# Optimization experiments

Measured on AMD Instinct MI355X. Metric: run time of the kernel, lower is better.

## Reference

```python
import jax, jax.numpy as jnp
import numpy as np

N, E, DIN, HID, DOUT = 50000, 800000, 128, 128, 64
NEG_SLOPE = 0.2


def setup_inputs() -> dict:
    key = jax.random.key(0)
    ks = jax.random.split(key, 16)
    x = jax.random.normal(ks[0], (N, DIN), dtype=jnp.float32)
    edge_index = jax.random.randint(ks[1], (2, E), 0, N, dtype=jnp.int64)

    def lin(k, fan_in, fan_out):
        kw, kb = jax.random.split(k)
        s = 1.0 / np.sqrt(fan_in)
        W = jax.random.uniform(kw, (fan_in, fan_out), jnp.float32, -s, s)
        b = jax.random.uniform(kb, (fan_out,), jnp.float32, -s, s)
        return W, b

    Wl, bl = lin(ks[2], DIN, DIN)   # GATv2 lin_l
    Wr, br = lin(ks[3], DIN, DIN)   # GATv2 lin_r
    att = jax.random.uniform(ks[4], (DIN,), jnp.float32, -1.0 / np.sqrt(DIN), 1.0 / np.sqrt(DIN))
    bg = jnp.zeros((DIN,), jnp.float32)  # GAT output bias
    W1, b1 = lin(ks[5], DIN, HID)   # ChebConv K=1 -> plain linear
    W2, b2 = lin(ks[6], HID, HID)
    W3, b3 = lin(ks[7], HID, DOUT)
    return {"x": x, "edge_index": edge_index, "Wl": Wl, "bl": bl, "Wr": Wr,
            "br": br, "att": att, "bg": bg, "W1": W1, "b1": b1,
            "W2": W2, "b2": b2, "W3": W3, "b3": b3}


def reference(x, edge_index, Wl, bl, Wr, br, att, bg, W1, b1, W2, b2, W3, b3):
    n = x.shape[0]
    # GATv2Conv adds self loops by default
    loop = jnp.arange(n, dtype=edge_index.dtype)
    src = jnp.concatenate([edge_index[0], loop])  # source j
    dst = jnp.concatenate([edge_index[1], loop])  # target i

    xl = x @ Wl + bl  # [N, DIN]
    xr = x @ Wr + br  # [N, DIN]

    # GATv2 edge scores: leaky_relu(x_l[j] + x_r[i]) . att
    e = jax.nn.leaky_relu(xl[src] + xr[dst], NEG_SLOPE)  # [E+N, DIN]
    a = e @ att                                          # [E+N]

    # softmax over incoming edges of each destination node
    amax = jax.ops.segment_max(a, dst, num_segments=n)
    ea = jnp.exp(a - amax[dst])
    denom = jax.ops.segment_sum(ea, dst, num_segments=n)
    alpha = ea / denom[dst]                              # [E+N]

    # aggregate messages alpha * x_l[j] at destinations
    h = jax.ops.segment_sum(alpha[:, None] * xl[src], dst, num_segments=n) + bg

    # ChebConv with K=1 reduces to a linear layer (T_0(L) = I)
    h = jax.nn.relu(h @ W1 + b1)
    h = jax.nn.relu(h @ W2 + b2)
    # dropout_rate = 0.0 -> identity
    return h @ W3 + b3
```

## Files before the change

### kernel.cpp

```cpp
#include <hip/hip_runtime.h>
#include <hip/hip_bf16.h>

#define DIN 128
#define NEG_SLOPE 0.2f
#define PTILE 2048
#define FCAP 8192
#define CVT_BLKS 289

typedef __attribute__((ext_vector_type(8))) short bf16x8;
typedef __attribute__((ext_vector_type(8))) unsigned short u16x8;
typedef __attribute__((ext_vector_type(4))) float f32x4;

__device__ __forceinline__ ushort f2bf(float f) {
  unsigned u = __float_as_uint(f);
  u += 0x7FFFu + ((u >> 16) & 1u);
  return (ushort)(u >> 16);
}
__device__ __forceinline__ float bf2f(ushort u) {
  return __uint_as_float((unsigned)u << 16);
}

__global__ __launch_bounds__(256) void cvt_hist_kernel(
    const float* __restrict__ Wl, const float* __restrict__ Wr,
    const float* __restrict__ W1, const float* __restrict__ W2,
    const float* __restrict__ W3,
    ushort* __restrict__ WlT, ushort* __restrict__ WrT,
    ushort* __restrict__ W1T, ushort* __restrict__ W2T,
    ushort* __restrict__ W3T,
    const int* __restrict__ ei, int* __restrict__ ghist, int E) {
  if (blockIdx.x < CVT_BLKS) {
    int i = blockIdx.x * 256 + threadIdx.x;
    if (i < 16384) {
      int k = i >> 7, c = i & 127; WlT[c * 128 + k] = f2bf(Wl[i]);
    } else if (i < 32768) {
      int j = i - 16384; int k = j >> 7, c = j & 127; WrT[c * 128 + k] = f2bf(Wr[j]);
    } else if (i < 49152) {
      int j = i - 32768; int k = j >> 7, c = j & 127; W1T[c * 128 + k] = f2bf(W1[j]);
    } else if (i < 65536) {
      int j = i - 49152; int k = j >> 7, c = j & 127; W2T[c * 128 + k] = f2bf(W2[j]);
    } else if (i < 73728) {
      int j = i - 65536; int k = j >> 6, c = j & 63; W3T[c * 128 + k] = f2bf(W3[j]);
    }
  } else {
    __shared__ int h[256];
    h[threadIdx.x] = 0;
    __syncthreads();
    int tile = blockIdx.x - CVT_BLKS;
    for (int e = tile * PTILE + threadIdx.x;
         e < min(E, (tile + 1) * PTILE); e += 256)
      atomicAdd(&h[ei[E + e] >> 8], 1);
    __syncthreads();
    if (h[threadIdx.x] > 0) atomicAdd(&ghist[threadIdx.x], h[threadIdx.x]);
  }
}

__global__ __launch_bounds__(256) void lin_lr_mfma_kernel(
    const float* __restrict__ x,
    const ushort* __restrict__ WlT, const float* __restrict__ bl,
    const ushort* __restrict__ WrT, const float* __restrict__ br,
    ushort* __restrict__ xl, ushort* __restrict__ xr, int n) {
  const int tid = threadIdx.x;
  const int wv = tid >> 6, lane = tid & 63;
  const int m = lane & 15, quad = lane >> 4;
  const int colbase = (wv & 1) * 64;
  const int nodew = blockIdx.x * 32 + (wv >> 1) * 16;
  int arow = nodew + m; if (arow >= n) arow = n - 1;
  f32x4 accl[4], accr[4];
#pragma unroll
  for (int nt = 0; nt < 4; nt++) { accl[nt] = (f32x4){0,0,0,0}; accr[nt] = (f32x4){0,0,0,0}; }
#pragma unroll
  for (int kk = 0; kk < 4; kk++) {
    int k0 = kk * 32 + quad * 8;
    const float4* xp = (const float4*)(x + (long)arow * 128 + k0);
    float4 x0 = xp[0], x1 = xp[1];
    bf16x8 af;
    af[0] = (short)f2bf(x0.x); af[1] = (short)f2bf(x0.y);
    af[2] = (short)f2bf(x0.z); af[3] = (short)f2bf(x0.w);
    af[4] = (short)f2bf(x1.x); af[5] = (short)f2bf(x1.y);
    af[6] = (short)f2bf(x1.z); af[7] = (short)f2bf(x1.w);
#pragma unroll
    for (int nt = 0; nt < 4; nt++) {
      int brow = colbase + nt * 16 + m;
      bf16x8 bl8 = *(const bf16x8*)(WlT + brow * 128 + k0);
      bf16x8 br8 = *(const bf16x8*)(WrT + brow * 128 + k0);
      accl[nt] = __builtin_amdgcn_mfma_f32_16x16x32_bf16(af, bl8, accl[nt], 0, 0, 0);
      accr[nt] = __builtin_amdgcn_mfma_f32_16x16x32_bf16(af, br8, accr[nt], 0, 0, 0);
    }
  }
#pragma unroll
  for (int nt = 0; nt < 4; nt++) {
    int col = colbase + nt * 16 + m;
    float vbl = bl[col], vbr = br[col];
#pragma unroll
    for (int r = 0; r < 4; r++) {
      int node = nodew + quad * 4 + r;
      if (node < n) {
        xl[(long)node * 128 + col] = f2bf(accl[nt][r] + vbl);
        xr[(long)node * 128 + col] = f2bf(accr[nt][r] + vbr);
      }
    }
  }
}

__global__ __launch_bounds__(256) void scan_small_kernel(
    const int* __restrict__ ghist, int* __restrict__ cum,
    int* __restrict__ cursor) {
  __shared__ int sh[256];
  int tid = threadIdx.x;
  int v = ghist[tid];
  sh[tid] = v;
  __syncthreads();
  for (int d = 1; d < 256; d <<= 1) {
    int t = (tid >= d) ? sh[tid - d] : 0;
    __syncthreads();
    sh[tid] += t;
    __syncthreads();
  }
  int exc = sh[tid] - v;
  cum[tid] = exc;
  cursor[tid] = exc;
  if (tid == 255) cum[256] = sh[255];
}

__global__ __launch_bounds__(256) void partition_kernel(
    const int* __restrict__ ei, unsigned* __restrict__ part,
    int* __restrict__ cursor, int E) {
  __shared__ int hist[256], pref[256], sexcl[256], curs[256], gbase[256];
  __shared__ unsigned buf[PTILE];
  const int tid = threadIdx.x;
  const int tile0 = blockIdx.x * PTILE;
  const int tcount = min(PTILE, E - tile0);
  hist[tid] = 0;
  __syncthreads();
  unsigned pk[PTILE / 256];
  int cnt = 0;
  for (int i = tid; i < tcount; i += 256) {
    int e = tile0 + i;
    int s = ei[e], d = ei[E + e];
    unsigned p = ((unsigned)d << 16) | (unsigned)s;
    pk[cnt++] = p;
    atomicAdd(&hist[d >> 8], 1);
  }
  __syncthreads();
  int v = hist[tid];
  pref[tid] = v;
  __syncthreads();
  for (int d = 1; d < 256; d <<= 1) {
    int t = (tid >= d) ? pref[tid - d] : 0;
    __syncthreads();
    pref[tid] += t;
    __syncthreads();
  }
  int exc = pref[tid] - v;
  sexcl[tid] = exc;
  curs[tid] = exc;
  gbase[tid] = (v > 0) ? atomicAdd(&cursor[tid], v) : 0;
  __syncthreads();
  for (int j = 0; j < cnt; j++) {
    int b = pk[j] >> 24;
    int pos = atomicAdd(&curs[b], 1);
    buf[pos] = pk[j];
  }
  __syncthreads();
  for (int i = tid; i < tcount; i += 256) {
    unsigned p = buf[i];
    int b = p >> 24;
    part[gbase[b] + (i - sexcl[b])] = p;
  }
}

__global__ __launch_bounds__(512) void fine_kernel(
    const unsigned* __restrict__ part, const int* __restrict__ cum,
    int* __restrict__ offsets, int* __restrict__ ssrc,
    int N, int E, int nbuck) {
  __shared__ int hist[256], pref[256], curs[256];
  __shared__ unsigned buf[FCAP], buf2[FCAP];
  const int tid = threadIdx.x;
  const int b = blockIdx.x;
  const int seg0 = cum[b];
  const int len = min(cum[b + 1] - seg0, FCAP);
  if (tid < 256) hist[tid] = 0;
  __syncthreads();
  for (int i = tid; i < len; i += 512) {
    unsigned p = part[seg0 + i];
    buf[i] = p;
    atomicAdd(&hist[(p >> 16) & 255], 1);
  }
  __syncthreads();
  int v = (tid < 256) ? hist[tid] : 0;
  if (tid < 256) pref[tid] = v;
  __syncthreads();
  for (int d = 1; d < 256; d <<= 1) {
    int t = (tid >= d && tid < 256) ? pref[tid - d] : 0;
    __syncthreads();
    if (tid < 256) pref[tid] += t;
    __syncthreads();
  }
  if (tid < 256) {
    int exc = pref[tid] - v;
    curs[tid] = exc;
    int node = b * 256 + tid;
    if (node < N) offsets[node] = seg0 + exc;
  }
  if (b == nbuck - 1 && tid == 0) offsets[N] = E;
  __syncthreads();
  for (int i = tid; i < len; i += 512) {
    unsigned p = buf[i];
    int pos = atomicAdd(&curs[(p >> 16) & 255], 1);
    buf2[pos] = p;
  }
  __syncthreads();
  for (int i = tid; i < len; i += 512)
    ssrc[seg0 + i] = (int)(buf2[i] & 0xFFFFu);
}

__global__ __launch_bounds__(256) void node_aggr_kernel(
    const ushort* __restrict__ xl, const ushort* __restrict__ xr,
    const float* __restrict__ att, const float* __restrict__ bg,
    const int* __restrict__ offsets, const int* __restrict__ ssrc,
    ushort* __restrict__ h, int n) {
  int wave = (int)((blockIdx.x * (long)blockDim.x + threadIdx.x) >> 6);
  int lane = threadIdx.x & 63;
  if (wave >= n) return;
  const int node = wave;
  const int eg = lane >> 4, sl = lane & 15;
  float av[8], r[8], acc[8];
  {
    const float4* ap = (const float4*)(att + sl * 8);
    float4 a0 = ap[0], a1 = ap[1];
    av[0]=a0.x; av[1]=a0.y; av[2]=a0.z; av[3]=a0.w;
    av[4]=a1.x; av[5]=a1.y; av[6]=a1.z; av[7]=a1.w;
  }
  bf16x8 rv = *(const bf16x8*)(xr + (long)node * 128 + sl * 8);
#pragma unroll
  for (int j = 0; j < 8; j++) r[j] = bf2f((ushort)rv[j]);
  bf16x8 lv = *(const bf16x8*)(xl + (long)node * 128 + sl * 8);
  float denom;
  {
    float t = 0.f;
    float l[8];
#pragma unroll
    for (int j = 0; j < 8; j++) {
      l[j] = bf2f((ushort)lv[j]);
      float v = l[j] + r[j];
      v = fmaxf(v, NEG_SLOPE * v);
      t = fmaf(v, av[j], t);
    }
#pragma unroll
    for (int off = 1; off < 16; off <<= 1) t += __shfl_xor(t, off);
    float es = __expf(t);
    denom = (eg == 0) ? es : 0.f;
#pragma unroll
    for (int j = 0; j < 8; j++) acc[j] = (eg == 0) ? es * l[j] : 0.f;
  }
  const int beg = offsets[node];
  const int end = offsets[node + 1];
  for (int p = beg; p < end; p += 8) {
    int ia = p + eg, ib = p + 4 + eg;
    bool va = ia < end, vb = ib < end;
    int sa = va ? ssrc[ia] : node;
    int sb = vb ? ssrc[ib] : node;
    bf16x8 uva = *(const bf16x8*)(xl + (long)sa * 128 + sl * 8);
    bf16x8 uvb = *(const bf16x8*)(xl + (long)sb * 128 + sl * 8);
    float ua[8], ub[8], ta = 0.f, tb = 0.f;
#pragma unroll
    for (int j = 0; j < 8; j++) {
      ua[j] = bf2f((ushort)uva[j]);
      ub[j] = bf2f((ushort)uvb[j]);
      float wa = ua[j] + r[j]; wa = fmaxf(wa, NEG_SLOPE * wa);
      float wb = ub[j] + r[j]; wb = fmaxf(wb, NEG_SLOPE * wb);
      ta = fmaf(wa, av[j], ta);
      tb = fmaf(wb, av[j], tb);
    }
#pragma unroll
    for (int off = 1; off < 16; off <<= 1) {
      ta += __shfl_xor(ta, off);
      tb += __shfl_xor(tb, off);
    }
    float ea = va ? __expf(ta) : 0.f;
    float eb = vb ? __expf(tb) : 0.f;
    denom += ea + eb;
#pragma unroll
    for (int j = 0; j < 8; j++)
      acc[j] = fmaf(eb, ub[j], fmaf(ea, ua[j], acc[j]));
  }
#pragma unroll
  for (int j = 0; j < 8; j++) {
    acc[j] += __shfl_xor(acc[j], 16);
    acc[j] += __shfl_xor(acc[j], 32);
  }
  denom += __shfl_xor(denom, 16);
  denom += __shfl_xor(denom, 32);
  if (eg == 0) {
    float inv = 1.0f / denom;
    const float4* bp = (const float4*)(bg + sl * 8);
    float4 g0 = bp[0], g1 = bp[1];
    float gv[8] = {g0.x, g0.y, g0.z, g0.w, g1.x, g1.y, g1.z, g1.w};
    u16x8 o;
#pragma unroll
    for (int j = 0; j < 8; j++) o[j] = f2bf(fmaf(acc[j], inv, gv[j]));
    *(u16x8*)(h + (long)node * 128 + sl * 8) = o;
  }
}

#define LDSP 136
__global__ __launch_bounds__(256) void mlp_mfma_kernel(
    const ushort* __restrict__ hb,
    const ushort* __restrict__ W1T, const float* __restrict__ b1,
    const ushort* __restrict__ W2T, const float* __restrict__ b2,
    const ushort* __restrict__ W3T, const float* __restrict__ b3,
    float* __restrict__ out, int n) {
  __shared__ ushort act[32][LDSP];
  const int tid = threadIdx.x;
  const int wv = tid >> 6, lane = tid & 63;
  const int m = lane & 15, quad = lane >> 4;
  const int half = wv & 1, ng = wv >> 1;
  const int colbase = half * 64;
  const int nodew = blockIdx.x * 32 + ng * 16;
  int arow = nodew + m; if (arow >= n) arow = n - 1;
  f32x4 acc[4];
#pragma unroll
  for (int nt = 0; nt < 4; nt++) acc[nt] = (f32x4){0,0,0,0};
#pragma unroll
  for (int kk = 0; kk < 4; kk++) {
    int k0 = kk * 32 + quad * 8;
    bf16x8 af = *(const bf16x8*)(hb + (long)arow * 128 + k0);
#pragma unroll
    for (int nt = 0; nt < 4; nt++) {
      bf16x8 b8 = *(const bf16x8*)(W1T + (colbase + nt * 16 + m) * 128 + k0);
      acc[nt] = __builtin_amdgcn_mfma_f32_16x16x32_bf16(af, b8, acc[nt], 0, 0, 0);
    }
  }
#pragma unroll
  for (int nt = 0; nt < 4; nt++) {
    int col = colbase + nt * 16 + m;
    float b = b1[col];
#pragma unroll
    for (int r = 0; r < 4; r++)
      act[ng * 16 + quad * 4 + r][col] = f2bf(fmaxf(acc[nt][r] + b, 0.f));
  }
  __syncthreads();
#pragma unroll
  for (int nt = 0; nt < 4; nt++) acc[nt] = (f32x4){0,0,0,0};
#pragma unroll
  for (int kk = 0; kk < 4; kk++) {
    int k0 = kk * 32 + quad * 8;
    bf16x8 af = *(const bf16x8*)(&act[ng * 16 + m][k0]);
#pragma unroll
    for (int nt = 0; nt < 4; nt++) {
      bf16x8 b8 = *(const bf16x8*)(W2T + (colbase + nt * 16 + m) * 128 + k0);
      acc[nt] = __builtin_amdgcn_mfma_f32_16x16x32_bf16(af, b8, acc[nt], 0, 0, 0);
    }
  }
  __syncthreads();
#pragma unroll
  for (int nt = 0; nt < 4; nt++) {
    int col = colbase + nt * 16 + m;
    float b = b2[col];
#pragma unroll
    for (int r = 0; r < 4; r++)
      act[ng * 16 + quad * 4 + r][col] = f2bf(fmaxf(acc[nt][r] + b, 0.f));
  }
  __syncthreads();
  f32x4 acc3[2];
#pragma unroll
  for (int nt = 0; nt < 2; nt++) acc3[nt] = (f32x4){0,0,0,0};
#pragma unroll
  for (int kk = 0; kk < 4; kk++) {
    int k0 = kk * 32 + quad * 8;
    bf16x8 af = *(const bf16x8*)(&act[ng * 16 + m][k0]);
#pragma unroll
    for (int nt = 0; nt < 2; nt++) {
      bf16x8 b8 = *(const bf16x8*)(W3T + (half * 32 + nt * 16 + m) * 128 + k0);
      acc3[nt] = __builtin_amdgcn_mfma_f32_16x16x32_bf16(af, b8, acc3[nt], 0, 0, 0);
    }
  }
#pragma unroll
  for (int nt = 0; nt < 2; nt++) {
    int col = half * 32 + nt * 16 + m;
    float b = b3[col];
#pragma unroll
    for (int r = 0; r < 4; r++) {
      int node = nodew + quad * 4 + r;
      if (node < n) out[(long)node * 64 + col] = acc3[nt][r] + b;
    }
  }
}

extern "C" void kernel_launch(void* const* d_in, const int* in_sizes, int n_in,
                              void* d_out, int out_size, void* d_ws, size_t ws_size,
                              hipStream_t stream) {
  const float* x   = (const float*)d_in[0];
  const int*   ei  = (const int*)d_in[1];
  const float* Wl  = (const float*)d_in[2];
  const float* bl  = (const float*)d_in[3];
  const float* Wr  = (const float*)d_in[4];
  const float* br  = (const float*)d_in[5];
  const float* att = (const float*)d_in[6];
  const float* bg  = (const float*)d_in[7];
  const float* W1  = (const float*)d_in[8];
  const float* b1  = (const float*)d_in[9];
  const float* W2  = (const float*)d_in[10];
  const float* b2  = (const float*)d_in[11];
  const float* W3  = (const float*)d_in[12];
  const float* b3  = (const float*)d_in[13];
  float* out = (float*)d_out;

  const int N = in_sizes[0] / DIN;
  const int E = in_sizes[1] / 2;
  const int nbuck = (N + 255) >> 8;

  char* ws = (char*)d_ws;
  size_t off = 0;
  int* ghist    = (int*)(ws + off);    off += 256 * 4;
  int* cum      = (int*)(ws + off);    off += 257 * 4;
  int* cursor   = (int*)(ws + off);    off += 256 * 4;
  int* offsets  = (int*)(ws + off);    off += ((size_t)N + 4) * 4;
  unsigned* part= (unsigned*)(ws + off); off += (size_t)E * 4;
  int* ssrc     = (int*)(ws + off);    off += (size_t)E * 4;
  ushort* xlb   = (ushort*)(ws + off); off += (size_t)N * DIN * 2;
  ushort* xrb   = (ushort*)(ws + off); off += (size_t)N * DIN * 2;
  ushort* hbf   = (ushort*)(ws + off); off += (size_t)N * DIN * 2;
  ushort* WlT   = (ushort*)(ws + off); off += 16384 * 2;
  ushort* WrT   = (ushort*)(ws + off); off += 16384 * 2;
  ushort* W1T   = (ushort*)(ws + off); off += 16384 * 2;
  ushort* W2T   = (ushort*)(ws + off); off += 16384 * 2;
  ushort* W3T   = (ushort*)(ws + off); off += 8192 * 2;
  (void)ws_size;

  hipMemsetAsync(ghist, 0, 256 * 4, stream);

  int ntile = (E + PTILE - 1) / PTILE;
  cvt_hist_kernel<<<CVT_BLKS + ntile, 256, 0, stream>>>(
      Wl, Wr, W1, W2, W3, WlT, WrT, W1T, W2T, W3T, ei, ghist, E);

  int nblk32 = (N + 31) / 32;
  lin_lr_mfma_kernel<<<nblk32, 256, 0, stream>>>(x, WlT, bl, WrT, br,
                                                 xlb, xrb, N);

  scan_small_kernel<<<1, 256, 0, stream>>>(ghist, cum, cursor);
  partition_kernel<<<ntile, 256, 0, stream>>>(ei, part, cursor, E);
  fine_kernel<<<nbuck, 512, 0, stream>>>(part, cum, offsets, ssrc, N, E, nbuck);

  int nwblk = (N + 3) / 4;
  node_aggr_kernel<<<nwblk, 256, 0, stream>>>(xlb, xrb, att, bg,
                                              offsets, ssrc, hbf, N);

  mlp_mfma_kernel<<<nblk32, 256, 0, stream>>>(hbf, W1T, b1, W2T, b2,
                                              W3T, b3, out, N);
}
```

Measured before the change: 251.7 us.

## Fuse linear projection with edge partition; shrink source indices; pack aggregation math

Merges the GATv2 lin_l/lin_r MFMA kernel and the edge partition kernel into one launch, with block ranges split by index, so the two independent jobs run concurrently and one launch is removed. Sorted source indices are stored as 16-bit values instead of 32-bit, halving that traffic in fine_kernel and node_aggr. The aggregation kernel converts bf16 in pairs, uses two-wide float vector arithmetic, and has each 16-lane edge group take two consecutive edges. The workspace allocator now aligns every buffer to 256 bytes; the 16-bit indices assume N is at most 65536.

Result: faster. 242.1 us (-3.8%).

```diff
diff --git a/kernel.cpp b/kernel.cpp
--- a/kernel.cpp
+++ b/kernel.cpp
@@ -10,6 +10,8 @@
 typedef __attribute__((ext_vector_type(8))) short bf16x8;
 typedef __attribute__((ext_vector_type(8))) unsigned short u16x8;
 typedef __attribute__((ext_vector_type(4))) float f32x4;
+typedef __attribute__((ext_vector_type(2))) float f32x2;
+typedef __attribute__((ext_vector_type(4))) unsigned int u32x4;
 
 __device__ __forceinline__ ushort f2bf(float f) {
   unsigned u = __float_as_uint(f);
@@ -18,6 +20,12 @@
 }
 __device__ __forceinline__ float bf2f(ushort u) {
   return __uint_as_float((unsigned)u << 16);
+}
+__device__ __forceinline__ f32x2 bfpair(unsigned u) {
+  f32x2 r;
+  r.x = __uint_as_float(u << 16);
+  r.y = __uint_as_float(u & 0xFFFF0000u);
+  return r;
 }
 
 __global__ __launch_bounds__(256) void cvt_hist_kernel(
@@ -54,54 +62,6 @@
   }
 }
 
-__global__ __launch_bounds__(256) void lin_lr_mfma_kernel(
-    const float* __restrict__ x,
-    const ushort* __restrict__ WlT, const float* __restrict__ bl,
-    const ushort* __restrict__ WrT, const float* __restrict__ br,
-    ushort* __restrict__ xl, ushort* __restrict__ xr, int n) {
-  const int tid = threadIdx.x;
-  const int wv = tid >> 6, lane = tid & 63;
-  const int m = lane & 15, quad = lane >> 4;
-  const int colbase = (wv & 1) * 64;
-  const int nodew = blockIdx.x * 32 + (wv >> 1) * 16;
-  int arow = nodew + m; if (arow >= n) arow = n - 1;
-  f32x4 accl[4], accr[4];
-#pragma unroll
-  for (int nt = 0; nt < 4; nt++) { accl[nt] = (f32x4){0,0,0,0}; accr[nt] = (f32x4){0,0,0,0}; }
-#pragma unroll
-  for (int kk = 0; kk < 4; kk++) {
-    int k0 = kk * 32 + quad * 8;
-    const float4* xp = (const float4*)(x + (long)arow * 128 + k0);
-    float4 x0 = xp[0], x1 = xp[1];
-    bf16x8 af;
-    af[0] = (short)f2bf(x0.x); af[1] = (short)f2bf(x0.y);
-    af[2] = (short)f2bf(x0.z); af[3] = (short)f2bf(x0.w);
-    af[4] = (short)f2bf(x1.x); af[5] = (short)f2bf(x1.y);
-    af[6] = (short)f2bf(x1.z); af[7] = (short)f2bf(x1.w);
-#pragma unroll
-    for (int nt = 0; nt < 4; nt++) {
-      int brow = colbase + nt * 16 + m;
-      bf16x8 bl8 = *(const bf16x8*)(WlT + brow * 128 + k0);
-      bf16x8 br8 = *(const bf16x8*)(WrT + brow * 128 + k0);
-      accl[nt] = __builtin_amdgcn_mfma_f32_16x16x32_bf16(af, bl8, accl[nt], 0, 0, 0);
-      accr[nt] = __builtin_amdgcn_mfma_f32_16x16x32_bf16(af, br8, accr[nt], 0, 0, 0);
-    }
-  }
-#pragma unroll
-  for (int nt = 0; nt < 4; nt++) {
-    int col = colbase + nt * 16 + m;
-    float vbl = bl[col], vbr = br[col];
-#pragma unroll
-    for (int r = 0; r < 4; r++) {
-      int node = nodew + quad * 4 + r;
-      if (node < n) {
-        xl[(long)node * 128 + col] = f2bf(accl[nt][r] + vbl);
-        xr[(long)node * 128 + col] = f2bf(accr[nt][r] + vbr);
-      }
-    }
-  }
-}
-
 __global__ __launch_bounds__(256) void scan_small_kernel(
     const int* __restrict__ ghist, int* __restrict__ cum,
     int* __restrict__ cursor) {
@@ -122,56 +82,104 @@
   if (tid == 255) cum[256] = sh[255];
 }
 
-__global__ __launch_bounds__(256) void partition_kernel(
+__global__ __launch_bounds__(256) void lin_partition_kernel(
+    const float* __restrict__ x,
+    const ushort* __restrict__ WlT, const float* __restrict__ bl,
+    const ushort* __restrict__ WrT, const float* __restrict__ br,
+    ushort* __restrict__ xl, ushort* __restrict__ xr, int n, int nblk_lin,
     const int* __restrict__ ei, unsigned* __restrict__ part,
     int* __restrict__ cursor, int E) {
-  __shared__ int hist[256], pref[256], sexcl[256], curs[256], gbase[256];
-  __shared__ unsigned buf[PTILE];
-  const int tid = threadIdx.x;
-  const int tile0 = blockIdx.x * PTILE;
-  const int tcount = min(PTILE, E - tile0);
-  hist[tid] = 0;
-  __syncthreads();
-  unsigned pk[PTILE / 256];
-  int cnt = 0;
-  for (int i = tid; i < tcount; i += 256) {
-    int e = tile0 + i;
-    int s = ei[e], d = ei[E + e];
-    unsigned p = ((unsigned)d << 16) | (unsigned)s;
-    pk[cnt++] = p;
-    atomicAdd(&hist[d >> 8], 1);
-  }
-  __syncthreads();
-  int v = hist[tid];
-  pref[tid] = v;
-  __syncthreads();
-  for (int d = 1; d < 256; d <<= 1) {
-    int t = (tid >= d) ? pref[tid - d] : 0;
-    __syncthreads();
-    pref[tid] += t;
-    __syncthreads();
-  }
-  int exc = pref[tid] - v;
-  sexcl[tid] = exc;
-  curs[tid] = exc;
-  gbase[tid] = (v > 0) ? atomicAdd(&cursor[tid], v) : 0;
-  __syncthreads();
-  for (int j = 0; j < cnt; j++) {
-    int b = pk[j] >> 24;
-    int pos = atomicAdd(&curs[b], 1);
-    buf[pos] = pk[j];
-  }
-  __syncthreads();
-  for (int i = tid; i < tcount; i += 256) {
-    unsigned p = buf[i];
-    int b = p >> 24;
-    part[gbase[b] + (i - sexcl[b])] = p;
+  if ((int)blockIdx.x < nblk_lin) {
+    const int tid = threadIdx.x;
+    const int wv = tid >> 6, lane = tid & 63;
+    const int m = lane & 15, quad = lane >> 4;
+    const int colbase = (wv & 1) * 64;
+    const int nodew = blockIdx.x * 32 + (wv >> 1) * 16;
+    int arow = nodew + m; if (arow >= n) arow = n - 1;
+    f32x4 accl[4], accr[4];
+#pragma unroll
+    for (int nt = 0; nt < 4; nt++) { accl[nt] = (f32x4){0,0,0,0}; accr[nt] = (f32x4){0,0,0,0}; }
+#pragma unroll
+    for (int kk = 0; kk < 4; kk++) {
+      int k0 = kk * 32 + quad * 8;
+      const float4* xp = (const float4*)(x + (long)arow * 128 + k0);
+      float4 x0 = xp[0], x1 = xp[1];
+      bf16x8 af;
+      af[0] = (short)f2bf(x0.x); af[1] = (short)f2bf(x0.y);
+      af[2] = (short)f2bf(x0.z); af[3] = (short)f2bf(x0.w);
+      af[4] = (short)f2bf(x1.x); af[5] = (short)f2bf(x1.y);
+      af[6] = (short)f2bf(x1.z); af[7] = (short)f2bf(x1.w);
+#pragma unroll
+      for (int nt = 0; nt < 4; nt++) {
+        int brow = colbase + nt * 16 + m;
+        bf16x8 bl8 = *(const bf16x8*)(WlT + brow * 128 + k0);
+        bf16x8 br8 = *(const bf16x8*)(WrT + brow * 128 + k0);
+        accl[nt] = __builtin_amdgcn_mfma_f32_16x16x32_bf16(af, bl8, accl[nt], 0, 0, 0);
+        accr[nt] = __builtin_amdgcn_mfma_f32_16x16x32_bf16(af, br8, accr[nt], 0, 0, 0);
+      }
+    }
+#pragma unroll
+    for (int nt = 0; nt < 4; nt++) {
+      int col = colbase + nt * 16 + m;
+      float vbl = bl[col], vbr = br[col];
+#pragma unroll
+      for (int r = 0; r < 4; r++) {
+        int node = nodew + quad * 4 + r;
+        if (node < n) {
+          xl[(long)node * 128 + col] = f2bf(accl[nt][r] + vbl);
+          xr[(long)node * 128 + col] = f2bf(accr[nt][r] + vbr);
+        }
+      }
+    }
+  } else {
+    __shared__ int hist[256], pref[256], sexcl[256], curs[256], gbase[256];
+    __shared__ unsigned buf[PTILE];
+    const int tid = threadIdx.x;
+    const int tile0 = ((int)blockIdx.x - nblk_lin) * PTILE;
+    const int tcount = min(PTILE, E - tile0);
+    hist[tid] = 0;
+    __syncthreads();
+    unsigned pk[PTILE / 256];
+    int cnt = 0;
+    for (int i = tid; i < tcount; i += 256) {
+      int e = tile0 + i;
+      int s = ei[e], d = ei[E + e];
+      unsigned p = ((unsigned)d << 16) | (unsigned)s;
+      pk[cnt++] = p;
+      atomicAdd(&hist[d >> 8], 1);
+    }
+    __syncthreads();
+    int v = hist[tid];
+    pref[tid] = v;
+    __syncthreads();
+    for (int d = 1; d < 256; d <<= 1) {
+      int t = (tid >= d) ? pref[tid - d] : 0;
+      __syncthreads();
+      pref[tid] += t;
+      __syncthreads();
+    }
+    int exc = pref[tid] - v;
+    sexcl[tid] = exc;
+    curs[tid] = exc;
+    gbase[tid] = (v > 0) ? atomicAdd(&cursor[tid], v) : 0;
+    __syncthreads();
+    for (int j = 0; j < cnt; j++) {
+      int b = pk[j] >> 24;
+      int pos = atomicAdd(&curs[b], 1);
+      buf[pos] = pk[j];
+    }
+    __syncthreads();
+    for (int i = tid; i < tcount; i += 256) {
+      unsigned p = buf[i];
+      int b = p >> 24;
+      part[gbase[b] + (i - sexcl[b])] = p;
+    }
   }
 }
 
 __global__ __launch_bounds__(512) void fine_kernel(
     const unsigned* __restrict__ part, const int* __restrict__ cum,
-    int* __restrict__ offsets, int* __restrict__ ssrc,
+    int* __restrict__ offsets, ushort* __restrict__ ssrc,
     int N, int E, int nbuck) {
   __shared__ int hist[256], pref[256], curs[256];
   __shared__ unsigned buf[FCAP], buf2[FCAP];
@@ -211,67 +219,69 @@
   }
   __syncthreads();
   for (int i = tid; i < len; i += 512)
-    ssrc[seg0 + i] = (int)(buf2[i] & 0xFFFFu);
+    ssrc[seg0 + i] = (ushort)(buf2[i] & 0xFFFFu);
 }
 
 __global__ __launch_bounds__(256) void node_aggr_kernel(
     const ushort* __restrict__ xl, const ushort* __restrict__ xr,
     const float* __restrict__ att, const float* __restrict__ bg,
-    const int* __restrict__ offsets, const int* __restrict__ ssrc,
+    const int* __restrict__ offsets, const ushort* __restrict__ ssrc,
     ushort* __restrict__ h, int n) {
   int wave = (int)((blockIdx.x * (long)blockDim.x + threadIdx.x) >> 6);
   int lane = threadIdx.x & 63;
   if (wave >= n) return;
   const int node = wave;
   const int eg = lane >> 4, sl = lane & 15;
-  float av[8], r[8], acc[8];
+  f32x2 av2[4], r2[4], acc2[4];
   {
     const float4* ap = (const float4*)(att + sl * 8);
     float4 a0 = ap[0], a1 = ap[1];
-    av[0]=a0.x; av[1]=a0.y; av[2]=a0.z; av[3]=a0.w;
-    av[4]=a1.x; av[5]=a1.y; av[6]=a1.z; av[7]=a1.w;
-  }
-  bf16x8 rv = *(const bf16x8*)(xr + (long)node * 128 + sl * 8);
-#pragma unroll
-  for (int j = 0; j < 8; j++) r[j] = bf2f((ushort)rv[j]);
-  bf16x8 lv = *(const bf16x8*)(xl + (long)node * 128 + sl * 8);
+    av2[0] = (f32x2){a0.x, a0.y}; av2[1] = (f32x2){a0.z, a0.w};
+    av2[2] = (f32x2){a1.x, a1.y}; av2[3] = (f32x2){a1.z, a1.w};
+  }
+  u32x4 rv = *(const u32x4*)(xr + (long)node * 128 + sl * 8);
+  u32x4 lv = *(const u32x4*)(xl + (long)node * 128 + sl * 8);
   float denom;
   {
-    float t = 0.f;
-    float l[8];
-#pragma unroll
-    for (int j = 0; j < 8; j++) {
-      l[j] = bf2f((ushort)lv[j]);
-      float v = l[j] + r[j];
-      v = fmaxf(v, NEG_SLOPE * v);
-      t = fmaf(v, av[j], t);
-    }
+    f32x2 t2 = {0.f, 0.f};
+    f32x2 l2[4];
+#pragma unroll
+    for (int jp = 0; jp < 4; jp++) {
+      r2[jp] = bfpair(rv[jp]);
+      l2[jp] = bfpair(lv[jp]);
+      f32x2 v = l2[jp] + r2[jp];
+      t2 += __builtin_elementwise_max(v, NEG_SLOPE * v) * av2[jp];
+    }
+    float t = t2.x + t2.y;
 #pragma unroll
     for (int off = 1; off < 16; off <<= 1) t += __shfl_xor(t, off);
     float es = __expf(t);
     denom = (eg == 0) ? es : 0.f;
 #pragma unroll
-    for (int j = 0; j < 8; j++) acc[j] = (eg == 0) ? es * l[j] : 0.f;
+    for (int jp = 0; jp < 4; jp++)
+      acc2[jp] = (eg == 0) ? es * l2[jp] : (f32x2){0.f, 0.f};
   }
   const int beg = offsets[node];
   const int end = offsets[node + 1];
   for (int p = beg; p < end; p += 8) {
-    int ia = p + eg, ib = p + 4 + eg;
-    bool va = ia < end, vb = ib < end;
-    int sa = va ? ssrc[ia] : node;
-    int sb = vb ? ssrc[ib] : node;
-    bf16x8 uva = *(const bf16x8*)(xl + (long)sa * 128 + sl * 8);
-    bf16x8 uvb = *(const bf16x8*)(xl + (long)sb * 128 + sl * 8);
-    float ua[8], ub[8], ta = 0.f, tb = 0.f;
-#pragma unroll
-    for (int j = 0; j < 8; j++) {
-      ua[j] = bf2f((ushort)uva[j]);
-      ub[j] = bf2f((ushort)uvb[j]);
-      float wa = ua[j] + r[j]; wa = fmaxf(wa, NEG_SLOPE * wa);
-      float wb = ub[j] + r[j]; wb = fmaxf(wb, NEG_SLOPE * wb);
-      ta = fmaf(wa, av[j], ta);
-      tb = fmaf(wb, av[j], tb);
-    }
+    int ia = p + 2 * eg;
+    bool va = ia < end, vb = ia + 1 < end;
+    int sa = va ? (int)ssrc[ia] : node;
+    int sb = vb ? (int)ssrc[ia + 1] : node;
+    u32x4 uva = *(const u32x4*)(xl + (long)sa * 128 + sl * 8);
+    u32x4 uvb = *(const u32x4*)(xl + (long)sb * 128 + sl * 8);
+    f32x2 ua2[4], ub2[4];
+    f32x2 ta2 = {0.f, 0.f}, tb2 = {0.f, 0.f};
+#pragma unroll
+    for (int jp = 0; jp < 4; jp++) {
+      ua2[jp] = bfpair(uva[jp]);
+      ub2[jp] = bfpair(uvb[jp]);
+      f32x2 va2 = ua2[jp] + r2[jp];
+      f32x2 vb2 = ub2[jp] + r2[jp];
+      ta2 += __builtin_elementwise_max(va2, NEG_SLOPE * va2) * av2[jp];
+      tb2 += __builtin_elementwise_max(vb2, NEG_SLOPE * vb2) * av2[jp];
+    }
+    float ta = ta2.x + ta2.y, tb = tb2.x + tb2.y;
 #pragma unroll
     for (int off = 1; off < 16; off <<= 1) {
       ta += __shfl_xor(ta, off);
@@ -281,13 +291,15 @@
     float eb = vb ? __expf(tb) : 0.f;
     denom += ea + eb;
 #pragma unroll
-    for (int j = 0; j < 8; j++)
-      acc[j] = fmaf(eb, ub[j], fmaf(ea, ua[j], acc[j]));
-  }
-#pragma unroll
-  for (int j = 0; j < 8; j++) {
-    acc[j] += __shfl_xor(acc[j], 16);
-    acc[j] += __shfl_xor(acc[j], 32);
+    for (int jp = 0; jp < 4; jp++)
+      acc2[jp] += ea * ua2[jp] + eb * ub2[jp];
+  }
+#pragma unroll
+  for (int jp = 0; jp < 4; jp++) {
+    acc2[jp].x += __shfl_xor(acc2[jp].x, 16);
+    acc2[jp].y += __shfl_xor(acc2[jp].y, 16);
+    acc2[jp].x += __shfl_xor(acc2[jp].x, 32);
+    acc2[jp].y += __shfl_xor(acc2[jp].y, 32);
   }
   denom += __shfl_xor(denom, 16);
   denom += __shfl_xor(denom, 32);
@@ -295,10 +307,14 @@
     float inv = 1.0f / denom;
     const float4* bp = (const float4*)(bg + sl * 8);
     float4 g0 = bp[0], g1 = bp[1];
-    float gv[8] = {g0.x, g0.y, g0.z, g0.w, g1.x, g1.y, g1.z, g1.w};
+    f32x2 gv[4] = {{g0.x, g0.y}, {g0.z, g0.w}, {g1.x, g1.y}, {g1.z, g1.w}};
     u16x8 o;
 #pragma unroll
-    for (int j = 0; j < 8; j++) o[j] = f2bf(fmaf(acc[j], inv, gv[j]));
+    for (int jp = 0; jp < 4; jp++) {
+      f32x2 hv = acc2[jp] * inv + gv[jp];
+      o[2 * jp]     = f2bf(hv.x);
+      o[2 * jp + 1] = f2bf(hv.y);
+    }
     *(u16x8*)(h + (long)node * 128 + sl * 8) = o;
   }
 }
@@ -412,20 +428,25 @@
 
   char* ws = (char*)d_ws;
   size_t off = 0;
-  int* ghist    = (int*)(ws + off);    off += 256 * 4;
-  int* cum      = (int*)(ws + off);    off += 257 * 4;
-  int* cursor   = (int*)(ws + off);    off += 256 * 4;
-  int* offsets  = (int*)(ws + off);    off += ((size_t)N + 4) * 4;
-  unsigned* part= (unsigned*)(ws + off); off += (size_t)E * 4;
-  int* ssrc     = (int*)(ws + off);    off += (size_t)E * 4;
-  ushort* xlb   = (ushort*)(ws + off); off += (size_t)N * DIN * 2;
-  ushort* xrb   = (ushort*)(ws + off); off += (size_t)N * DIN * 2;
-  ushort* hbf   = (ushort*)(ws + off); off += (size_t)N * DIN * 2;
-  ushort* WlT   = (ushort*)(ws + off); off += 16384 * 2;
-  ushort* WrT   = (ushort*)(ws + off); off += 16384 * 2;
-  ushort* W1T   = (ushort*)(ws + off); off += 16384 * 2;
-  ushort* W2T   = (ushort*)(ws + off); off += 16384 * 2;
-  ushort* W3T   = (ushort*)(ws + off); off += 8192 * 2;
+  auto alloc = [&](size_t bytes) {
+    void* p = ws + off;
+    off += (bytes + 255) & ~(size_t)255;
+    return p;
+  };
+  int* ghist     = (int*)alloc(256 * 4);
+  int* cum       = (int*)alloc(257 * 4);
+  int* cursor    = (int*)alloc(256 * 4);
+  int* offsets   = (int*)alloc(((size_t)N + 4) * 4);
+  unsigned* part = (unsigned*)alloc((size_t)E * 4);
+  ushort* ssrc   = (ushort*)alloc(((size_t)E + 16) * 2);
+  ushort* xlb    = (ushort*)alloc((size_t)N * DIN * 2);
+  ushort* xrb    = (ushort*)alloc((size_t)N * DIN * 2);
+  ushort* hbf    = (ushort*)alloc((size_t)N * DIN * 2);
+  ushort* WlT    = (ushort*)alloc(16384 * 2);
+  ushort* WrT    = (ushort*)alloc(16384 * 2);
+  ushort* W1T    = (ushort*)alloc(16384 * 2);
+  ushort* W2T    = (ushort*)alloc(16384 * 2);
+  ushort* W3T    = (ushort*)alloc(8192 * 2);
   (void)ws_size;
 
   hipMemsetAsync(ghist, 0, 256 * 4, stream);
@@ -434,12 +455,12 @@
   cvt_hist_kernel<<<CVT_BLKS + ntile, 256, 0, stream>>>(
       Wl, Wr, W1, W2, W3, WlT, WrT, W1T, W2T, W3T, ei, ghist, E);
 
+  scan_small_kernel<<<1, 256, 0, stream>>>(ghist, cum, cursor);
+
   int nblk32 = (N + 31) / 32;
-  lin_lr_mfma_kernel<<<nblk32, 256, 0, stream>>>(x, WlT, bl, WrT, br,
-                                                 xlb, xrb, N);
-
-  scan_small_kernel<<<1, 256, 0, stream>>>(ghist, cum, cursor);
-  partition_kernel<<<ntile, 256, 0, stream>>>(ei, part, cursor, E);
+  lin_partition_kernel<<<nblk32 + ntile, 256, 0, stream>>>(
+      x, WlT, bl, WrT, br, xlb, xrb, N, nblk32, ei, part, cursor, E);
+
   fine_kernel<<<nbuck, 512, 0, stream>>>(part, cum, offsets, ssrc, N, E, nbuck);
 
   int nwblk = (N + 3) / 4;
```
